# Optimization experiments

Measured on AMD Instinct MI355X. Metric: run time of the kernel, lower is better.

The kernel has to match this reference:

```python
import jax, jax.numpy as jnp
import numpy as np

SAMPLERATE = 22050
N_OCTAVES = 16
N_SAMPLES = 32768
MIN_FREQ = 20.0 / (SAMPLERATE // 2)
MAX_FREQ = 3000.0 / (SAMPLERATE // 2)
FREQ_RANGE = MAX_FREQ - MIN_FREQ
BASE_RESONANCE = 0.01


def max_norm(x, axis=-1, eps=1e-8):
    return x / (jnp.max(jnp.abs(x), axis=axis, keepdims=True) + eps)


def exponential_decay(decay_values, n_octaves):
    # decay_values: (B, E, 1). Note the original applies sigmoid here on top of
    # the sigmoid already applied in forward (sigmoid_decay=True) -> double sigmoid.
    dv = jax.nn.sigmoid(decay_values)  # (B, E, 1)
    resonance_factor = (1.0 - BASE_RESONANCE) * 0.99
    decay = BASE_RESONANCE + dv * resonance_factor  # (B, E, 1)
    logd = jnp.log(decay + 1e-12)
    b, e, _ = decay_values.shape
    # cumsum of a per-(b,e) constant over octaves, then exp (matches torch code;
    # F.interpolate to size==n_octaves is the identity here)
    logd = jnp.broadcast_to(logd, (b, e, n_octaves))
    return jnp.exp(jnp.cumsum(logd, axis=-1))  # (B, E, O)


def setup_inputs() -> dict:
    key = jax.random.key(0)
    k1, k2, k3 = jax.random.split(key, 3)
    B, E = 8, 64
    return {
        "f0": jax.random.uniform(k1, (B, E, 1), dtype=jnp.float32),
        "decay_coefficients": jax.random.normal(k2, (B, E, 1), dtype=jnp.float32),
        "unused": jnp.zeros((B, E, 1), dtype=jnp.float32),
        "freq_spacing": jax.random.uniform(k3, (B, E, 1), dtype=jnp.float32),
    }


def reference(f0, decay_coefficients, unused, freq_spacing):
    b, e, _ = f0.shape
    O, S = N_OCTAVES, N_SAMPLES

    f0 = jnp.abs(f0)  # (B, E, 1)
    # sigmoid_decay=True path: sigmoid applied before exponential_decay
    exp_decays = exponential_decay(jax.nn.sigmoid(decay_coefficients), O)  # (B, E, O)

    f0 = (MIN_FREQ + f0 * FREQ_RANGE) * jnp.pi  # (B, E, 1)

    # freq_spacing repeated over octaves then cumsum -> per-octave factors
    factors = jnp.cumsum(jnp.broadcast_to(freq_spacing, (b, e, O)), axis=-1)
    f0s = f0 * factors  # (B, E, O)

    # nyquist cutoff
    f0s = f0s * (f0s < 1.0)

    # phase: cumsum over samples of constant per-octave frequency (faithful to torch)
    phase = jnp.cumsum(jnp.broadcast_to(f0s[..., None], (b, e, O, S)), axis=-1)
    osc = jnp.sin(phase)  # (B, E, O, S)

    osc = osc * exp_decays[..., None]
    osc = jnp.sum(osc, axis=2)  # (B, E, S)
    return max_norm(osc, axis=-1)
```

## Files before the change

kernel.cpp:

```cpp
#include <hip/hip_runtime.h>
#include <hip/hip_fp16.h>
#include <math.h>

#define N_OCT 16
#define NPAIR 8
#define NS    32768
#define TPB   512
#define SPT   (NS / TPB)
#define N_BE  512

typedef float v2f __attribute__((ext_vector_type(2)));
typedef _Float16 h4 __attribute__((ext_vector_type(4)));

static __device__ __forceinline__ v2f fma2(v2f a, v2f b, v2f c) {
    return __builtin_elementwise_fma(a, b, c);
}

#define WS_R(ws)    ((double*)(ws))
#define WS_C2H(ws)  ((float*)((char*)(ws) + 65536))
#define WS_C2L(ws)  ((float*)((char*)(ws) + 98304))
#define WS_AMP(ws)  ((float*)((char*)(ws) + 131072))

__global__ __launch_bounds__(256)
void f0res_setup(const float* __restrict__ f0_in,
                 const float* __restrict__ dc_in,
                 const float* __restrict__ fs_in,
                 void* __restrict__ ws)
{
    const int idx = blockIdx.x * 256 + threadIdx.x;
    if (idx >= N_BE * N_OCT) return;
    const int be = idx >> 4, o = idx & 15;

    const float f0a = fabsf(f0_in[be]);
    const float dc  = dc_in[be];
    const float fs  = fs_in[be];

    const float MINF = (float)(20.0 / 11025.0);
    const float FRNG = (float)(3000.0 / 11025.0 - 20.0 / 11025.0);

    const float s1    = 1.0f / (1.0f + __expf(-dc));
    const float dv    = 1.0f / (1.0f + __expf(-s1));
    const float decay = 0.01f + dv * 0.9801f;
    const float logd  = __logf(decay + 1e-12f);
    const float f0r   = (MINF + f0a * FRNG) * 3.14159274101257324f;

    float cl = 0.f, cf = 0.f;
    for (int i = 0; i <= o; ++i) { cl += logd; cf += fs; }
    float ed  = __expf(cl);
    float f0s = f0r * cf;
    float a   = ed;
    if (!(f0s < 1.0f)) { a = 0.0f; f0s = 0.0f; }

    const double inv2pi = 0.15915494309189535;
    double r = (double)f0s * inv2pi;

    double drev = r * (double)TPB;
    drev -= floor(drev);
    double c2d = 2.0 * cos(drev * 6.283185307179586);
    float  ch  = (float)c2d;

    WS_R(ws)[idx]   = r;
    WS_C2H(ws)[idx] = ch;
    WS_C2L(ws)[idx] = (float)(c2d - (double)ch);
    WS_AMP(ws)[idx] = a;
}

__global__ __launch_bounds__(TPB, 1)
void f0res_kernel(const void* __restrict__ ws,
                  float* __restrict__ out)
{
    extern __shared__ _Float16 smem[];
    __shared__ float wmax[TPB / 64];

    const int be = blockIdx.x;
    const int t  = threadIdx.x;

    const double* __restrict__ Rtab = WS_R(ws)   + be * N_OCT;
    const float*  __restrict__ CH   = WS_C2H(ws) + be * N_OCT;
    const float*  __restrict__ CLo  = WS_C2L(ws) + be * N_OCT;
    const float*  __restrict__ AMP  = WS_AMP(ws) + be * N_OCT;

    v2f xp[NPAIR], xc[NPAIR], c2h[NPAIR], c2l[NPAIR];

    #pragma unroll
    for (int o = 0; o < N_OCT; ++o) {
        const double r = Rtab[o];
        const float  a = AMP[o];

        double p0 = r * (double)(t + 1);
        p0 -= floor(p0);
        double pm = r * (double)(t + 1 - TPB);
        pm -= floor(pm);
        float xcur  = a * __builtin_amdgcn_sinf((float)p0);
        float xprev = a * __builtin_amdgcn_sinf((float)pm);

        const int j = o >> 1;
        if ((o & 1) == 0) {
            xc[j].x = xcur;   xp[j].x = xprev;
            c2h[j].x = CH[o]; c2l[j].x = CLo[o];
        } else {
            xc[j].y = xcur;   xp[j].y = xprev;
            c2h[j].y = CH[o]; c2l[j].y = CLo[o];
        }
    }

    float lmax = 0.0f;
    #pragma unroll 4
    for (int k = 0; k < SPT; ++k) {
        v2f acc2 = (v2f)(0.0f);
        #pragma unroll
        for (int j = 0; j < NPAIR; ++j) {
            acc2 += xc[j];
            v2f xn = fma2(c2h[j], xc[j], fma2(c2l[j], xc[j], -xp[j]));
            xp[j] = xc[j];
            xc[j] = xn;
        }
        float acc = acc2.x + acc2.y;
        smem[k * TPB + t] = (_Float16)acc;
        lmax = fmaxf(lmax, fabsf(acc));
    }

    #pragma unroll
    for (int off = 32; off > 0; off >>= 1)
        lmax = fmaxf(lmax, __shfl_down(lmax, off, 64));
    if ((t & 63) == 0) wmax[t >> 6] = lmax;
    __syncthreads();
    float bmax = wmax[0];
    #pragma unroll
    for (int w = 1; w < TPB / 64; ++w) bmax = fmaxf(bmax, wmax[w]);

    const float norm = 1.0f / (bmax + 1e-8f);
    float4* out4 = (float4*)(out + (size_t)be * NS);
    #pragma unroll
    for (int j = 0; j < NS / 4 / TPB; ++j) {
        int i = j * TPB + t;
        h4 v = *(const h4*)(smem + 4 * (size_t)i);
        float4 o;
        o.x = (float)v.x * norm; o.y = (float)v.y * norm;
        o.z = (float)v.z * norm; o.w = (float)v.w * norm;
        out4[i] = o;
    }
}

extern "C" void kernel_launch(void* const* d_in, const int* in_sizes, int n_in,
                              void* d_out, int out_size, void* d_ws, size_t ws_size,
                              hipStream_t stream) {
    const float* f0 = (const float*)d_in[0];
    const float* dc = (const float*)d_in[1];
    const float* fs = (const float*)d_in[3];
    float* out = (float*)d_out;

    hipLaunchKernelGGL(f0res_setup, dim3((N_BE * N_OCT + 255) / 256), dim3(256),
                       0, stream, f0, dc, fs, d_ws);
    hipLaunchKernelGGL(f0res_kernel, dim3(N_BE), dim3(TPB),
                       NS * sizeof(_Float16), stream, d_ws, out);
}
```

Baseline: 99.68 us.

## Use 1024-thread blocks with scalar-broadcast recurrence coefficients and scalar FMAs

Block size doubles to 1024 threads, so each thread produces half as many samples. The recurrence coefficients are made wave-uniform with readfirstlane so they can sit in scalar registers, and the packed v2f math becomes scalar FMAs accumulated into four partial sums. The aim is to cut vector register pressure and shorten each thread's serial chain, at the cost of giving up packed FMA throughput and doing more per-thread sine initialisation overall.

```diff
diff --git a/kernel.cpp b/kernel.cpp
--- a/kernel.cpp
+++ b/kernel.cpp
@@ -3,17 +3,15 @@
 #include <math.h>
 
 #define N_OCT 16
-#define NPAIR 8
 #define NS    32768
-#define TPB   512
+#define TPB   1024
 #define SPT   (NS / TPB)
 #define N_BE  512
 
-typedef float v2f __attribute__((ext_vector_type(2)));
 typedef _Float16 h4 __attribute__((ext_vector_type(4)));
 
-static __device__ __forceinline__ v2f fma2(v2f a, v2f b, v2f c) {
-    return __builtin_elementwise_fma(a, b, c);
+static __device__ __forceinline__ float bcast0(float x) {
+    return __int_as_float(__builtin_amdgcn_readfirstlane(__float_as_int(x)));
 }
 
 #define WS_R(ws)    ((double*)(ws))
@@ -65,7 +63,7 @@
     WS_AMP(ws)[idx] = a;
 }
 
-__global__ __launch_bounds__(TPB, 1)
+__global__ __launch_bounds__(TPB)
 void f0res_kernel(const void* __restrict__ ws,
                   float* __restrict__ out)
 {
@@ -80,7 +78,8 @@
     const float*  __restrict__ CLo  = WS_C2L(ws) + be * N_OCT;
     const float*  __restrict__ AMP  = WS_AMP(ws) + be * N_OCT;
 
-    v2f xp[NPAIR], xc[NPAIR], c2h[NPAIR], c2l[NPAIR];
+    float xp[N_OCT], xc[N_OCT];
+    float c2h_s[N_OCT], c2l_s[N_OCT];
 
     #pragma unroll
     for (int o = 0; o < N_OCT; ++o) {
@@ -91,31 +90,29 @@
         p0 -= floor(p0);
         double pm = r * (double)(t + 1 - TPB);
         pm -= floor(pm);
-        float xcur  = a * __builtin_amdgcn_sinf((float)p0);
-        float xprev = a * __builtin_amdgcn_sinf((float)pm);
+        xc[o] = a * __builtin_amdgcn_sinf((float)p0);
+        xp[o] = a * __builtin_amdgcn_sinf((float)pm);
 
-        const int j = o >> 1;
-        if ((o & 1) == 0) {
-            xc[j].x = xcur;   xp[j].x = xprev;
-            c2h[j].x = CH[o]; c2l[j].x = CLo[o];
-        } else {
-            xc[j].y = xcur;   xp[j].y = xprev;
-            c2h[j].y = CH[o]; c2l[j].y = CLo[o];
-        }
+        c2h_s[o] = bcast0(CH[o]);
+        c2l_s[o] = bcast0(CLo[o]);
     }
 
     float lmax = 0.0f;
-    #pragma unroll 4
+    #pragma unroll 2
     for (int k = 0; k < SPT; ++k) {
-        v2f acc2 = (v2f)(0.0f);
+        float a0 = 0.f, a1 = 0.f, a2 = 0.f, a3 = 0.f;
         #pragma unroll
-        for (int j = 0; j < NPAIR; ++j) {
-            acc2 += xc[j];
-            v2f xn = fma2(c2h[j], xc[j], fma2(c2l[j], xc[j], -xp[j]));
-            xp[j] = xc[j];
-            xc[j] = xn;
+        for (int o = 0; o < N_OCT; ++o) {
+            float x = xc[o];
+            if ((o & 3) == 0) a0 += x;
+            else if ((o & 3) == 1) a1 += x;
+            else if ((o & 3) == 2) a2 += x;
+            else a3 += x;
+            float xn = fmaf(c2h_s[o], x, fmaf(c2l_s[o], x, -xp[o]));
+            xp[o] = x;
+            xc[o] = xn;
         }
-        float acc = acc2.x + acc2.y;
+        float acc = (a0 + a1) + (a2 + a3);
         smem[k * TPB + t] = (_Float16)acc;
         lmax = fmaxf(lmax, fabsf(acc));
     }
```

New measurement: 111.3 us. +11.7%, slower.

## Split per-row oscillator synthesis into chunked two-pass kernels with global max

Applied to the files above, without the earlier changes.

Each (batch, event) row is now split into four sample chunks processed by separate 256-thread blocks. Pass A runs the recurrence, writes fp16 partial results to global workspace, and atomically maxes the per-row peak. Pass B then normalizes and writes the float output. This raises block count and parallelism compared with one 512-thread block per row using 64KB of LDS. The cost is an extra kernel launch and a global fp16 round trip in place of LDS staging.

```diff
diff --git a/kernel.cpp b/kernel.cpp
--- a/kernel.cpp
+++ b/kernel.cpp
@@ -2,12 +2,15 @@
 #include <hip/hip_fp16.h>
 #include <math.h>
 
-#define N_OCT 16
-#define NPAIR 8
-#define NS    32768
-#define TPB   512
-#define SPT   (NS / TPB)
-#define N_BE  512
+#define N_OCT   16
+#define NPAIR   8
+#define NS      32768
+#define N_BE    512
+#define TPB_A   256
+#define NCHUNK  4
+#define CHUNK   (NS / NCHUNK)
+#define SPT_A   (CHUNK / TPB_A)
+#define STRIDE  TPB_A
 
 typedef float v2f __attribute__((ext_vector_type(2)));
 typedef _Float16 h4 __attribute__((ext_vector_type(4)));
@@ -20,6 +23,8 @@
 #define WS_C2H(ws)  ((float*)((char*)(ws) + 65536))
 #define WS_C2L(ws)  ((float*)((char*)(ws) + 98304))
 #define WS_AMP(ws)  ((float*)((char*)(ws) + 131072))
+#define WS_MAXU(ws) ((unsigned*)((char*)(ws) + 163840))
+#define WS_RAW(ws)  ((_Float16*)((char*)(ws) + 262144))
 
 __global__ __launch_bounds__(256)
 void f0res_setup(const float* __restrict__ f0_in,
@@ -30,6 +35,7 @@
     const int idx = blockIdx.x * 256 + threadIdx.x;
     if (idx >= N_BE * N_OCT) return;
     const int be = idx >> 4, o = idx & 15;
+    if (idx < N_BE) WS_MAXU(ws)[idx] = 0u;
 
     const float f0a = fabsf(f0_in[be]);
     const float dc  = dc_in[be];
@@ -54,7 +60,7 @@
     const double inv2pi = 0.15915494309189535;
     double r = (double)f0s * inv2pi;
 
-    double drev = r * (double)TPB;
+    double drev = r * (double)STRIDE;
     drev -= floor(drev);
     double c2d = 2.0 * cos(drev * 6.283185307179586);
     float  ch  = (float)c2d;
@@ -65,15 +71,15 @@
     WS_AMP(ws)[idx] = a;
 }
 
-__global__ __launch_bounds__(TPB, 1)
-void f0res_kernel(const void* __restrict__ ws,
-                  float* __restrict__ out)
+__global__ __launch_bounds__(TPB_A, 1)
+void f0res_passA(const void* __restrict__ ws)
 {
-    extern __shared__ _Float16 smem[];
-    __shared__ float wmax[TPB / 64];
+    __shared__ float wmax[TPB_A / 64];
 
-    const int be = blockIdx.x;
-    const int t  = threadIdx.x;
+    const int be    = blockIdx.x >> 2;
+    const int chunk = blockIdx.x & 3;
+    const int t     = threadIdx.x;
+    const int s0    = chunk * CHUNK + t;
 
     const double* __restrict__ Rtab = WS_R(ws)   + be * N_OCT;
     const float*  __restrict__ CH   = WS_C2H(ws) + be * N_OCT;
@@ -87,9 +93,9 @@
         const double r = Rtab[o];
         const float  a = AMP[o];
 
-        double p0 = r * (double)(t + 1);
+        double p0 = r * (double)(s0 + 1);
         p0 -= floor(p0);
-        double pm = r * (double)(t + 1 - TPB);
+        double pm = r * (double)(s0 + 1 - STRIDE);
         pm -= floor(pm);
         float xcur  = a * __builtin_amdgcn_sinf((float)p0);
         float xprev = a * __builtin_amdgcn_sinf((float)pm);
@@ -104,9 +110,11 @@
         }
     }
 
+    _Float16* __restrict__ raw = WS_RAW(ws) + (size_t)be * NS + chunk * CHUNK;
+
     float lmax = 0.0f;
     #pragma unroll 4
-    for (int k = 0; k < SPT; ++k) {
+    for (int k = 0; k < SPT_A; ++k) {
         v2f acc2 = (v2f)(0.0f);
         #pragma unroll
         for (int j = 0; j < NPAIR; ++j) {
@@ -116,7 +124,7 @@
             xc[j] = xn;
         }
         float acc = acc2.x + acc2.y;
-        smem[k * TPB + t] = (_Float16)acc;
+        raw[k * TPB_A + t] = (_Float16)acc;
         lmax = fmaxf(lmax, fabsf(acc));
     }
 
@@ -125,16 +133,34 @@
         lmax = fmaxf(lmax, __shfl_down(lmax, off, 64));
     if ((t & 63) == 0) wmax[t >> 6] = lmax;
     __syncthreads();
-    float bmax = wmax[0];
+    if (t == 0) {
+        float bmax = wmax[0];
+        #pragma unroll
+        for (int w = 1; w < TPB_A / 64; ++w) bmax = fmaxf(bmax, wmax[w]);
+        atomicMax(WS_MAXU(ws) + be, __float_as_uint(bmax));
+    }
+}
+
+__global__ __launch_bounds__(TPB_A)
+void f0res_passB(const void* __restrict__ ws,
+                 float* __restrict__ out)
+{
+    const int be    = blockIdx.x >> 2;
+    const int chunk = blockIdx.x & 3;
+    const int t     = threadIdx.x;
+
+    const float mx   = __uint_as_float(WS_MAXU(ws)[be]);
+    const float norm = 1.0f / (mx + 1e-8f);
+
+    const h4* __restrict__ raw4 =
+        (const h4*)(WS_RAW(ws) + (size_t)be * NS + chunk * CHUNK);
+    float4* __restrict__ out4 =
+        (float4*)(out + (size_t)be * NS + chunk * CHUNK);
+
     #pragma unroll
-    for (int w = 1; w < TPB / 64; ++w) bmax = fmaxf(bmax, wmax[w]);
-
-    const float norm = 1.0f / (bmax + 1e-8f);
-    float4* out4 = (float4*)(out + (size_t)be * NS);
-    #pragma unroll
-    for (int j = 0; j < NS / 4 / TPB; ++j) {
-        int i = j * TPB + t;
-        h4 v = *(const h4*)(smem + 4 * (size_t)i);
+    for (int j = 0; j < CHUNK / 4 / TPB_A; ++j) {
+        int i = j * TPB_A + t;
+        h4 v = raw4[i];
         float4 o;
         o.x = (float)v.x * norm; o.y = (float)v.y * norm;
         o.z = (float)v.z * norm; o.w = (float)v.w * norm;
@@ -150,8 +176,10 @@
     const float* fs = (const float*)d_in[3];
     float* out = (float*)d_out;
 
-    hipLaunchKernelGGL(f0res_setup, dim3((N_BE * N_OCT + 255) / 256), dim3(256),
+    hipLaunchKernelGGL(f0res_setup, dim3((N_BE * N_OCT) / 256), dim3(256),
                        0, stream, f0, dc, fs, d_ws);
-    hipLaunchKernelGGL(f0res_kernel, dim3(N_BE), dim3(TPB),
-                       NS * sizeof(_Float16), stream, d_ws, out);
+    hipLaunchKernelGGL(f0res_passA, dim3(N_BE * NCHUNK), dim3(TPB_A),
+                       0, stream, d_ws);
+    hipLaunchKernelGGL(f0res_passB, dim3(N_BE * NCHUNK), dim3(TPB_A),
+                       0, stream, d_ws, out);
 }
```

Result: slower. 117.3 us (+17.7%).
